# Kernel optimization log

Hardware: AMD Instinct MI355X
Metric: run time of the kernel (lower is better)

The kernel has to match this reference:

```python
import jax, jax.numpy as jnp
import numpy as np

B, F_IN, N, S = 2, 128, 192, 192   # batch, in_features, n_nodes, seq (seq==n_nodes required by mask broadcast)
H, D = 4, 64                        # n_heads, n_hidden (out_features = H*D = 256)
NEG_SLOPE = 0.2


def setup_inputs() -> dict:
    key = jax.random.key(0)
    ks = jax.random.split(key, 6)
    X = jax.random.normal(ks[0], (B, F_IN, N, S), dtype=jnp.float32)
    A = jax.random.randint(ks[1], (N, N, 1), 0, 2, dtype=jnp.int32)
    W_lin = jax.random.normal(ks[2], (F_IN, H * D), dtype=jnp.float32) * 0.05
    b_lin = jax.random.uniform(ks[3], (H * D,), dtype=jnp.float32)
    W_attn = jax.random.normal(ks[4], (2 * D,), dtype=jnp.float32) * 0.05
    b_attn = jax.random.uniform(ks[5], (1,), dtype=jnp.float32)
    return {"X": X, "A": A, "W_lin": W_lin, "b_lin": b_lin,
            "W_attn": W_attn, "b_attn": b_attn}


def reference(X, A, W_lin, b_lin, W_attn, b_attn):
    # Dropout is identity (eval mode).
    b, f, n, s = X.shape
    x = jnp.transpose(X, (0, 3, 2, 1))                      # (b, s, n, f)
    g = (x @ W_lin + b_lin).reshape(b, s, n, H, D)          # (b, s, n, H, D)
    # attn is affine: attn(cat[g_i, g_j]) = a_src.g_i + a_dst.g_j + b_attn
    a_src, a_dst = W_attn[:D], W_attn[D:]
    s_src = jnp.einsum('bsnhd,d->bsnh', g, a_src)
    s_dst = jnp.einsum('bsnhd,d->bsnh', g, a_dst)
    e = s_src[:, :, :, None, :] + s_dst[:, :, None, :, :] + b_attn[0]  # (b, s, n_i, n_j, H)
    e = jnp.where(e >= 0, e, NEG_SLOPE * e)                 # LeakyReLU
    # torch masked_fill broadcast: mask (n,n,1,1) aligns with e dims (s, n_i, n_j, H)
    e = jnp.where(A[..., None] == 0, -jnp.inf, e)
    alphas = jax.nn.softmax(e, axis=1)                      # softmax over seq dim (dim=1, as in source)
    alphas = jnp.nan_to_num(alphas, nan=0.0)
    # einsum 'mnojh,klphf->mnohf': independent sums over j (alphas) and k,l,p (g)
    sum_g = g.sum(axis=(0, 1, 2))                           # (H, D)
    attn_res = alphas.sum(axis=3)[..., None] * sum_g        # (b, s, n, H, D)
    out = attn_res.reshape(b, s, n, H * D)                  # concat=True
    return jnp.transpose(out, (0, 3, 2, 1))                 # (b, out_features, n, s)
```

## Files before the change

kernel.cpp:

```cpp
#include <hip/hip_runtime.h>
#include <math.h>

#define B_ 2
#define F_ 128
#define N_ 192
#define S_ 192
#define NS_ (N_ * S_)
#define LOG2E 1.4426950408889634f

#if defined(__has_builtin)
#if __has_builtin(__builtin_amdgcn_exp2f)
#define EXP2(x) __builtin_amdgcn_exp2f(x)
#else
#define EXP2(x) exp2f(x)
#endif
#else
#define EXP2(x) exp2f(x)
#endif

#define OFF_WSRC 0
#define OFF_WDST 512
#define OFF_CSRC 1024
#define OFF_CDST 1028
#define OFF_SUMG 1040
#define OFF_PART 1296
#define OFF_PE   2320
#define OFF_QD   (OFF_PE + 8 * NS_ * 2)
#define OFF_QT   (OFF_QD + 8 * NS_ * 2)

__global__ __launch_bounds__(256) void kPre(const float* __restrict__ X,
                                            const float* __restrict__ W_lin,
                                            const float* __restrict__ b_lin,
                                            const float* __restrict__ W_attn,
                                            const float* __restrict__ b_attn,
                                            float* __restrict__ ws) {
    int blk = blockIdx.x, t = threadIdx.x;
    if (blk < 1024) {
        int sq = blk & 3, f = (blk >> 2) & 127, b = blk >> 9;
        const float4* p = (const float4*)(X + ((size_t)(b * F_ + f)) * NS_ + sq * 9216);
        float acc = 0.f;
#pragma unroll
        for (int k = 0; k < 9; k++) {
            float4 v = p[t + k * 256];
            acc += (v.x + v.y) + (v.z + v.w);
        }
        for (int o = 32; o; o >>= 1) acc += __shfl_down(acc, o, 64);
        __shared__ float red[4];
        if ((t & 63) == 0) red[t >> 6] = acc;
        __syncthreads();
        if (t == 0)
            ws[OFF_PART + sq * 256 + b * 128 + f] = (red[0] + red[1]) + (red[2] + red[3]);
    } else if (blk == 1024) {
        const float4* wa = (const float4*)W_attn;
        for (int c = t; c < 512; c += 256) {
            int f = c >> 2, h = c & 3;
            const float4* wl = (const float4*)(W_lin + f * 256 + h * 64);
            float as = 0.f, ad = 0.f;
#pragma unroll
            for (int q = 0; q < 16; q++) {
                float4 w = wl[q], a1 = wa[q], a2 = wa[16 + q];
                as += w.x * a1.x + w.y * a1.y + w.z * a1.z + w.w * a1.w;
                ad += w.x * a2.x + w.y * a2.y + w.z * a2.z + w.w * a2.w;
            }
            ws[OFF_WSRC + c] = as * LOG2E;
            ws[OFF_WDST + c] = ad * LOG2E;
        }
    } else {
        if (t < 4) {
            float c = 0.f;
            for (int d = 0; d < 64; d++) c += b_lin[t * 64 + d] * W_attn[d];
            ws[OFF_CSRC + t] = (c + b_attn[0]) * LOG2E;
        } else if (t < 8) {
            int h = t - 4;
            float c = 0.f;
            for (int d = 0; d < 64; d++) c += b_lin[h * 64 + d] * W_attn[64 + d];
            ws[OFF_CDST + h] = c * LOG2E;
        }
    }
}

__global__ __launch_bounds__(256) void kProj(const float* __restrict__ X,
                                             const int* __restrict__ A,
                                             const float* __restrict__ W_lin,
                                             const float* __restrict__ b_lin,
                                             float* __restrict__ ws) {
    __shared__ float4 wsl[128], wdl[128];
    __shared__ float red[4 * 64 * 9];
    __shared__ float xs[128];
    __shared__ float wbuf[4096];
    int t = threadIdx.x, blk = blockIdx.x;
    if (blk < 1152) {
        int n = blk % 192, bsc = blk / 192;
        int b = bsc / 3, sc = bsc % 3;
        if (t < 128) {
            wsl[t] = ((const float4*)(ws + OFF_WSRC))[t];
            wdl[t] = ((const float4*)(ws + OFF_WDST))[t];
        }
        __syncthreads();
        int fq = t >> 6, lane = t & 63;
        int s = sc * 64 + lane;
        float aS[4] = {0, 0, 0, 0}, aD[4] = {0, 0, 0, 0};
        const float* xp = X + (size_t)(b * F_) * NS_ + n * S_ + s;
        int f0 = fq * 32;
#pragma unroll 8
        for (int fi = 0; fi < 32; fi++) {
            float x = xp[(size_t)(f0 + fi) * NS_];
            float4 w1 = wsl[f0 + fi], w2 = wdl[f0 + fi];
            aS[0] += x * w1.x; aS[1] += x * w1.y; aS[2] += x * w1.z; aS[3] += x * w1.w;
            aD[0] += x * w2.x; aD[1] += x * w2.y; aD[2] += x * w2.z; aD[3] += x * w2.w;
        }
        float* rp = red + t * 9;
#pragma unroll
        for (int h = 0; h < 4; h++) { rp[h] = aS[h]; rp[4 + h] = aD[h]; }
        __syncthreads();
        float2* PEp = (float2*)(ws + OFF_PE);
        float2* QD2 = (float2*)(ws + OFF_QD);
        float2* QT2 = (float2*)(ws + OFF_QT);
#pragma unroll
        for (int c = t; c < 512; c += 256) {
            int s_loc = c >> 3, k = c & 7;
            float v = red[s_loc * 9 + k] + red[(64 + s_loc) * 9 + k] +
                      red[(128 + s_loc) * 9 + k] + red[(192 + s_loc) * 9 + k];
            int ss = sc * 64 + s_loc;
            if (k < 4) {
                int bh = b * 4 + k;
                bool masked = (A[ss * 192 + n] == 0);
                float2 pr; pr.x = 0.f; pr.y = 0.f;
                if (!masked) {
                    float pt = v + ws[OFF_CSRC + k];
                    pr.x = EXP2(pt); pr.y = EXP2(0.2f * pt);
                }
                PEp[(size_t)bh * NS_ + n * 192 + ss] = pr;
            } else {
                int h = k - 4, bh = b * 4 + h;
                float dv = v + ws[OFF_CDST + h];
                float2 qr; qr.x = EXP2(dv); qr.y = EXP2(0.2f * dv);
                QD2[(size_t)bh * NS_ + ss * 192 + n] = qr;
                QT2[(size_t)bh * NS_ + n * 192 + ss] = qr;
            }
        }
    } else {
        if (t < 128) {
            float v = 0.f;
#pragma unroll
            for (int q = 0; q < 8; q++) v += ws[OFF_PART + q * 128 + t];
            xs[t] = v;
        }
        float acc = 0.f;
        for (int ch = 0; ch < 8; ch++) {
            const float4* s4 = (const float4*)(W_lin + ch * 4096);
            __syncthreads();
#pragma unroll
            for (int k = 0; k < 4; k++) ((float4*)wbuf)[t + k * 256] = s4[t + k * 256];
            __syncthreads();
#pragma unroll
            for (int fi = 0; fi < 16; fi++) acc += xs[ch * 16 + fi] * wbuf[fi * 256 + t];
        }
        ws[OFF_SUMG + t] = acc + 73728.f * b_lin[t];
    }
}

__global__ __launch_bounds__(384) void kAttn(const float* __restrict__ ws,
                                             float* __restrict__ out) {
    int blk = blockIdx.x, t = threadIdx.x;
    int bh = blk & 7, iq = blk >> 3;
    int b = bh >> 2, h = bh & 3;
    __shared__ float4 pe4[192];
    __shared__ float zpart[4 * 2 * 192];
    __shared__ float2 zr2[192];
    __shared__ float accp[4 * 2 * 192];
    __shared__ float sg_sh[64];
    const float2* PEp = (const float2*)(ws + OFF_PE) + (size_t)bh * NS_;
    const float4* QD4 = (const float4*)(ws + OFF_QD) + (size_t)bh * (NS_ / 2);
    const float4* QT4 = (const float4*)(ws + OFF_QT) + (size_t)bh * (NS_ / 2);
    if (t < 64) sg_sh[t] = ws[OFF_SUMG + h * 64 + t];
    if (t < 192) {
        float2 e0 = PEp[(iq * 2) * 192 + t];
        float2 e1 = PEp[(iq * 2 + 1) * 192 + t];
        pe4[t] = make_float4(e0.x, e0.y, e1.x, e1.y);
    }
    __syncthreads();

    {
        int sq = t / 96, jp = t - sq * 96;
        float z00 = 0.f, z01 = 0.f, z10 = 0.f, z11 = 0.f;
#pragma unroll 8
        for (int s = sq * 48; s < sq * 48 + 48; s++) {
            float4 q = QD4[s * 96 + jp];
            float4 E = pe4[s];
            z00 += fmaxf(E.x * q.x, E.y * q.y);
            z01 += fmaxf(E.x * q.z, E.y * q.w);
            z10 += fmaxf(E.z * q.x, E.w * q.y);
            z11 += fmaxf(E.z * q.z, E.w * q.w);
        }
        float* zp = zpart + sq * 384;
        zp[2 * jp] = z00; zp[2 * jp + 1] = z01;
        zp[192 + 2 * jp] = z10; zp[192 + 2 * jp + 1] = z11;
    }
    __syncthreads();
    {
        int r = t / 192, j = t - r * 192;
        float Z = zpart[r * 192 + j] + zpart[384 + r * 192 + j] +
                  zpart[768 + r * 192 + j] + zpart[1152 + r * 192 + j];
        ((float*)zr2)[j * 2 + r] = (Z != 0.f) ? (1.f / Z) : 0.f;
    }
    __syncthreads();

    {
        int jq = t / 96, sp = t - jq * 96;
        int s0 = 2 * sp, s1 = 2 * sp + 1;
        float4 E0 = pe4[s0], E1 = pe4[s1];
        float a00 = 0.f, a01 = 0.f, a10 = 0.f, a11 = 0.f;
#pragma unroll 8
        for (int j = jq * 48; j < jq * 48 + 48; j++) {
            float4 g = QT4[j * 96 + sp];
            float2 zr = zr2[j];
            a00 += fmaxf(E0.x * g.x, E0.y * g.y) * zr.x;
            a01 += fmaxf(E1.x * g.z, E1.y * g.w) * zr.x;
            a10 += fmaxf(E0.z * g.x, E0.w * g.y) * zr.y;
            a11 += fmaxf(E1.z * g.z, E1.w * g.w) * zr.y;
        }
        float* ap = accp + jq * 384;
        ap[s0] = a00; ap[s1] = a01;
        ap[192 + s0] = a10; ap[192 + s1] = a11;
    }
    __syncthreads();

    {
        int r = t / 192, s = t - r * 192;
        float acc = accp[r * 192 + s] + accp[384 + r * 192 + s] +
                    accp[768 + r * 192 + s] + accp[1152 + r * 192 + s];
        int i = iq * 2 + r;
        float* op = out + (((size_t)(b * 256 + h * 64)) * 192 + i) * 192 + s;
#pragma unroll 8
        for (int d = 0; d < 64; d++)
            op[(size_t)d * NS_] = acc * sg_sh[d];
    }
}

extern "C" void kernel_launch(void* const* d_in, const int* in_sizes, int n_in,
                              void* d_out, int out_size, void* d_ws, size_t ws_size,
                              hipStream_t stream) {
    const float* X      = (const float*)d_in[0];
    const int*   A      = (const int*)d_in[1];
    const float* W_lin  = (const float*)d_in[2];
    const float* b_lin  = (const float*)d_in[3];
    const float* W_attn = (const float*)d_in[4];
    const float* b_attn = (const float*)d_in[5];
    float* out = (float*)d_out;
    float* ws  = (float*)d_ws;

    kPre<<<1026, 256, 0, stream>>>(X, W_lin, b_lin, W_attn, b_attn, ws);
    kProj<<<1153, 256, 0, stream>>>(X, A, W_lin, b_lin, ws);
    kAttn<<<768, 384, 0, stream>>>(ws, out);
}
```

Before: 156.7 us.

## Assign attention work items dynamically by XCC-local queues for L2 locality

```diff
diff --git a/kernel.cpp b/kernel.cpp
--- a/kernel.cpp
+++ b/kernel.cpp
@@ -7,6 +7,8 @@
 #define S_ 192
 #define NS_ (N_ * S_)
 #define LOG2E 1.4426950408889634f
+#define AGENT __HIP_MEMORY_SCOPE_AGENT
+#define XCC_GETREG_IMM (20 | (7 << 11))
 
 #if defined(__has_builtin)
 #if __has_builtin(__builtin_amdgcn_exp2f)
@@ -27,6 +29,9 @@
 #define OFF_PE   2320
 #define OFF_QD   (OFF_PE + 8 * NS_ * 2)
 #define OFF_QT   (OFF_QD + 8 * NS_ * 2)
+
+__device__ int g_q[8];
+__device__ int g_exit;
 
 __global__ __launch_bounds__(256) void kPre(const float* __restrict__ X,
                                             const float* __restrict__ W_lin,
@@ -162,79 +167,105 @@
 
 __global__ __launch_bounds__(384) void kAttn(const float* __restrict__ ws,
                                              float* __restrict__ out) {
-    int blk = blockIdx.x, t = threadIdx.x;
-    int bh = blk & 7, iq = blk >> 3;
-    int b = bh >> 2, h = bh & 3;
-    __shared__ float4 pe4[192];
-    __shared__ float zpart[4 * 2 * 192];
-    __shared__ float2 zr2[192];
-    __shared__ float accp[4 * 2 * 192];
-    __shared__ float sg_sh[64];
-    const float2* PEp = (const float2*)(ws + OFF_PE) + (size_t)bh * NS_;
-    const float4* QD4 = (const float4*)(ws + OFF_QD) + (size_t)bh * (NS_ / 2);
-    const float4* QT4 = (const float4*)(ws + OFF_QT) + (size_t)bh * (NS_ / 2);
-    if (t < 64) sg_sh[t] = ws[OFF_SUMG + h * 64 + t];
-    if (t < 192) {
-        float2 e0 = PEp[(iq * 2) * 192 + t];
-        float2 e1 = PEp[(iq * 2 + 1) * 192 + t];
-        pe4[t] = make_float4(e0.x, e0.y, e1.x, e1.y);
+    int t = threadIdx.x;
+    __shared__ int sh_bh, sh_iq;
+    if (t == 0) {
+        int pref = (int)(__builtin_amdgcn_s_getreg(XCC_GETREG_IMM)) & 7;
+        int gb = 0, gi = -1;
+        for (int k = 0; k < 8; k++) {
+            int q = (pref + k) & 7;
+            int v = __hip_atomic_fetch_add(&g_q[q], 1, __ATOMIC_RELAXED, AGENT);
+            if (v < 96) { gb = q; gi = v; break; }
+        }
+        sh_bh = gb; sh_iq = gi;
     }
     __syncthreads();
-
-    {
-        int sq = t / 96, jp = t - sq * 96;
-        float z00 = 0.f, z01 = 0.f, z10 = 0.f, z11 = 0.f;
-#pragma unroll 8
-        for (int s = sq * 48; s < sq * 48 + 48; s++) {
-            float4 q = QD4[s * 96 + jp];
-            float4 E = pe4[s];
-            z00 += fmaxf(E.x * q.x, E.y * q.y);
-            z01 += fmaxf(E.x * q.z, E.y * q.w);
-            z10 += fmaxf(E.z * q.x, E.w * q.y);
-            z11 += fmaxf(E.z * q.z, E.w * q.w);
-        }
-        float* zp = zpart + sq * 384;
-        zp[2 * jp] = z00; zp[2 * jp + 1] = z01;
-        zp[192 + 2 * jp] = z10; zp[192 + 2 * jp + 1] = z11;
-    }
+    int bh = sh_bh, iq = sh_iq;
+
+    if (iq >= 0) {
+        int b = bh >> 2, h = bh & 3;
+        __shared__ float4 pe4[192];
+        __shared__ float zpart[4 * 2 * 192];
+        __shared__ float2 zr2[192];
+        __shared__ float accp[4 * 2 * 192];
+        __shared__ float sg_sh[64];
+        const float2* PEp = (const float2*)(ws + OFF_PE) + (size_t)bh * NS_;
+        const float4* QD4 = (const float4*)(ws + OFF_QD) + (size_t)bh * (NS_ / 2);
+        const float4* QT4 = (const float4*)(ws + OFF_QT) + (size_t)bh * (NS_ / 2);
+        if (t < 64) sg_sh[t] = ws[OFF_SUMG + h * 64 + t];
+        if (t < 192) {
+            float2 e0 = PEp[(iq * 2) * 192 + t];
+            float2 e1 = PEp[(iq * 2 + 1) * 192 + t];
+            pe4[t] = make_float4(e0.x, e0.y, e1.x, e1.y);
+        }
+        __syncthreads();
+
+        {
+            int sq = t / 96, jp = t - sq * 96;
+            float z00 = 0.f, z01 = 0.f, z10 = 0.f, z11 = 0.f;
+#pragma unroll 8
+            for (int s = sq * 48; s < sq * 48 + 48; s++) {
+                float4 q = QD4[s * 96 + jp];
+                float4 E = pe4[s];
+                z00 += fmaxf(E.x * q.x, E.y * q.y);
+                z01 += fmaxf(E.x * q.z, E.y * q.w);
+                z10 += fmaxf(E.z * q.x, E.w * q.y);
+                z11 += fmaxf(E.z * q.z, E.w * q.w);
+            }
+            float* zp = zpart + sq * 384;
+            zp[2 * jp] = z00; zp[2 * jp + 1] = z01;
+            zp[192 + 2 * jp] = z10; zp[192 + 2 * jp + 1] = z11;
+        }
+        __syncthreads();
+        {
+            int r = t / 192, j = t - r * 192;
+            float Z = zpart[r * 192 + j] + zpart[384 + r * 192 + j] +
+                      zpart[768 + r * 192 + j] + zpart[1152 + r * 192 + j];
+            ((float*)zr2)[j * 2 + r] = (Z != 0.f) ? (1.f / Z) : 0.f;
+        }
+        __syncthreads();
+
+        {
+            int jq = t / 96, sp = t - jq * 96;
+            int s0 = 2 * sp, s1 = 2 * sp + 1;
+            float4 E0 = pe4[s0], E1 = pe4[s1];
+            float a00 = 0.f, a01 = 0.f, a10 = 0.f, a11 = 0.f;
+#pragma unroll 8
+            for (int j = jq * 48; j < jq * 48 + 48; j++) {
+                float4 g = QT4[j * 96 + sp];
+                float2 zr = zr2[j];
+                a00 += fmaxf(E0.x * g.x, E0.y * g.y) * zr.x;
+                a01 += fmaxf(E1.x * g.z, E1.y * g.w) * zr.x;
+                a10 += fmaxf(E0.z * g.x, E0.w * g.y) * zr.y;
+                a11 += fmaxf(E1.z * g.z, E1.w * g.w) * zr.y;
+            }
+            float* ap = accp + jq * 384;
+            ap[s0] = a00; ap[s1] = a01;
+            ap[192 + s0] = a10; ap[192 + s1] = a11;
+        }
+        __syncthreads();
+
+        {
+            int r = t / 192, s = t - r * 192;
+            float acc = accp[r * 192 + s] + accp[384 + r * 192 + s] +
+                        accp[768 + r * 192 + s] + accp[1152 + r * 192 + s];
+            int i = iq * 2 + r;
+            float* op = out + (((size_t)(b * 256 + h * 64)) * 192 + i) * 192 + s;
+#pragma unroll 8
+            for (int d = 0; d < 64; d++)
+                op[(size_t)d * NS_] = acc * sg_sh[d];
+        }
+    }
+
     __syncthreads();
-    {
-        int r = t / 192, j = t - r * 192;
-        float Z = zpart[r * 192 + j] + zpart[384 + r * 192 + j] +
-                  zpart[768 + r * 192 + j] + zpart[1152 + r * 192 + j];
-        ((float*)zr2)[j * 2 + r] = (Z != 0.f) ? (1.f / Z) : 0.f;
-    }
-    __syncthreads();
-
-    {
-        int jq = t / 96, sp = t - jq * 96;
-        int s0 = 2 * sp, s1 = 2 * sp + 1;
-        float4 E0 = pe4[s0], E1 = pe4[s1];
-        float a00 = 0.f, a01 = 0.f, a10 = 0.f, a11 = 0.f;
-#pragma unroll 8
-        for (int j = jq * 48; j < jq * 48 + 48; j++) {
-            float4 g = QT4[j * 96 + sp];
-            float2 zr = zr2[j];
-            a00 += fmaxf(E0.x * g.x, E0.y * g.y) * zr.x;
-            a01 += fmaxf(E1.x * g.z, E1.y * g.w) * zr.x;
-            a10 += fmaxf(E0.z * g.x, E0.w * g.y) * zr.y;
-            a11 += fmaxf(E1.z * g.z, E1.w * g.w) * zr.y;
-        }
-        float* ap = accp + jq * 384;
-        ap[s0] = a00; ap[s1] = a01;
-        ap[192 + s0] = a10; ap[192 + s1] = a11;
-    }
-    __syncthreads();
-
-    {
-        int r = t / 192, s = t - r * 192;
-        float acc = accp[r * 192 + s] + accp[384 + r * 192 + s] +
-                    accp[768 + r * 192 + s] + accp[1152 + r * 192 + s];
-        int i = iq * 2 + r;
-        float* op = out + (((size_t)(b * 256 + h * 64)) * 192 + i) * 192 + s;
-#pragma unroll 8
-        for (int d = 0; d < 64; d++)
-            op[(size_t)d * NS_] = acc * sg_sh[d];
+    if (t == 0) {
+        int e = __hip_atomic_fetch_add(&g_exit, 1, __ATOMIC_ACQ_REL, AGENT);
+        if (e == 767) {
+#pragma unroll
+            for (int i = 0; i < 8; i++)
+                __hip_atomic_store(&g_q[i], 0, __ATOMIC_RELAXED, AGENT);
+            __hip_atomic_store(&g_exit, 0, __ATOMIC_RELEASE, AGENT);
+        }
     }
 }
 
```

New measurement: 174.6 us. +11.5%, slower.
